# Optimization experiments

Hardware: AMD Instinct MI355X
Metric: run time of the kernel (lower is better)

The kernel has to match this reference:

```python
import jax, jax.numpy as jnp
import numpy as np

B, S, D_MODEL = 2, 2048, 2048
H, DS, DG, DV = 16, 64, 64, 128
ROPE_BASE = 10000.0
NEG_INF = -1e9


def _rope(x, base=ROPE_BASE):
    # x: [B, S, H, D] -> rotate-half RoPE over positions 0..S-1
    d = x.shape[-1]
    half = d // 2
    inv_freq = 1.0 / (base ** (jnp.arange(half, dtype=jnp.float32) / half))
    ang = jnp.arange(x.shape[1], dtype=jnp.float32)[:, None] * inv_freq  # [S, half]
    cos = jnp.cos(ang)[None, :, None, :]
    sin = jnp.sin(ang)[None, :, None, :]
    x1, x2 = x[..., :half], x[..., half:]
    return jnp.concatenate([x1 * cos - x2 * sin, x1 * sin + x2 * cos], axis=-1)


def setup_inputs() -> dict:
    key = jax.random.key(0)
    ks = jax.random.split(key, 8)
    s = lambda fan_in: 1.0 / np.sqrt(fan_in)
    return {
        "x": jax.random.normal(ks[0], (B, S, D_MODEL), dtype=jnp.float32),
        "wq_sem": jax.random.normal(ks[1], (D_MODEL, H * DS), dtype=jnp.float32) * s(D_MODEL),
        "wk_sem": jax.random.normal(ks[2], (D_MODEL, H * DS), dtype=jnp.float32) * s(D_MODEL),
        "wq_geo": jax.random.normal(ks[3], (D_MODEL, H * DG), dtype=jnp.float32) * s(D_MODEL),
        "wk_geo": jax.random.normal(ks[4], (D_MODEL, H * DG), dtype=jnp.float32) * s(D_MODEL),
        "wv": jax.random.normal(ks[5], (D_MODEL, H * DV), dtype=jnp.float32) * s(D_MODEL),
        "wo": jax.random.normal(ks[6], (H * DV, D_MODEL), dtype=jnp.float32) * s(H * DV),
        "gate_logit": jax.random.normal(ks[7], (H,), dtype=jnp.float32),
    }


def reference(x, wq_sem, wk_sem, wq_geo, wk_geo, wv, wo, gate_logit):
    b, sl, _ = x.shape
    # Projections -> [B, S, H, d]
    qs = (x @ wq_sem).reshape(b, sl, H, DS)
    ksem = (x @ wk_sem).reshape(b, sl, H, DS)
    qg = _rope((x @ wq_geo).reshape(b, sl, H, DG))
    kg = _rope((x @ wk_geo).reshape(b, sl, H, DG))
    v = (x @ wv).reshape(b, sl, H, DV)

    sem_scale = 1.0 / np.sqrt(DS)
    geo_scale = 1.0 / np.sqrt(DG)
    sem_scores = jnp.einsum("bqhd,bkhd->bhqk", qs, ksem) * sem_scale
    geo_scores = jnp.einsum("bqhd,bkhd->bhqk", qg, kg) * geo_scale

    # Learned per-head gate mixing semantic vs geometric paths
    g = jax.nn.sigmoid(gate_logit)[None, :, None, None]
    scores = g * sem_scores + (1.0 - g) * geo_scores

    causal = jnp.tril(jnp.ones((sl, sl), dtype=bool))
    scores = jnp.where(causal[None, None], scores, NEG_INF)
    attn = jax.nn.softmax(scores, axis=-1)

    out = jnp.einsum("bhqk,bkhd->bqhd", attn, v).reshape(b, sl, H * DV)
    return out @ wo
```

## Files before the change

### kernel.cpp

```cpp
#include <hip/hip_runtime.h>
#include <hip/hip_bf16.h>

typedef unsigned short u16;
typedef __attribute__((ext_vector_type(4))) float floatx4;
typedef __attribute__((ext_vector_type(8))) __bf16 bf16x8;

__device__ __forceinline__ u16 f2bf(float f) {
  unsigned int x = __builtin_bit_cast(unsigned int, f);
  unsigned int r = (x + 0x7fffu + ((x >> 16) & 1u)) >> 16;
  return (u16)r;
}
__device__ __forceinline__ float bf2f(u16 u) {
  unsigned int x = ((unsigned int)u) << 16;
  return __builtin_bit_cast(float, x);
}
__device__ __forceinline__ floatx4 mfma16(bf16x8 a, bf16x8 b, floatx4 c) {
  return __builtin_amdgcn_mfma_f32_16x16x32_bf16(a, b, c, 0, 0, 0);
}
__device__ __forceinline__ void gload16(const u16* g, u16* l) {
  __builtin_amdgcn_global_load_lds(
      (const __attribute__((address_space(1))) unsigned int*)g,
      (__attribute__((address_space(3))) unsigned int*)l, 16, 0, 0);
}
#define SCHEDB() __builtin_amdgcn_sched_barrier(0)
#define SBAR() __builtin_amdgcn_s_barrier()

#define BB 2
#define SS 2048
#define DM 2048
#define HH 16
#define PCOLS 6144

__global__ void convert_bf16_k(const float* __restrict__ src, u16* __restrict__ dst, size_t n) {
  size_t i = ((size_t)blockIdx.x * blockDim.x + threadIdx.x) * 4;
  if (i + 3 >= n) { for (size_t j = i; j < n; ++j) dst[j] = f2bf(src[j]); return; }
  float4 v = *(const float4*)&src[i];
  ushort4 o; o.x = f2bf(v.x); o.y = f2bf(v.y); o.z = f2bf(v.z); o.w = f2bf(v.w);
  *(ushort4*)&dst[i] = o;
}

__global__ void transpose_all_k(const float* w0, const float* w1, const float* w2,
                                const float* w3, const float* w4, const float* w5,
                                u16* __restrict__ WcatT, u16* __restrict__ WoT) {
  __shared__ float tile[32][33];
  const int z = blockIdx.z;
  const float* src; u16* dst; int cols;
  if (z == 0)      { src = w0; dst = WcatT;                        cols = 1024; }
  else if (z == 1) { src = w1; dst = WcatT + (size_t)1024 * 2048;  cols = 1024; }
  else if (z == 2) { src = w2; dst = WcatT + (size_t)2048 * 2048;  cols = 1024; }
  else if (z == 3) { src = w3; dst = WcatT + (size_t)3072 * 2048;  cols = 1024; }
  else if (z == 4) { src = w4; dst = WcatT + (size_t)4096 * 2048;  cols = 2048; }
  else             { src = w5; dst = WoT;                          cols = 2048; }
  int c0 = blockIdx.x * 32;
  if (c0 >= cols) return;
  int r0 = blockIdx.y * 32;
  int tx = threadIdx.x, ty = threadIdx.y;
#pragma unroll
  for (int i = 0; i < 4; ++i)
    tile[ty + i * 8][tx] = src[(size_t)(r0 + ty + i * 8) * cols + c0 + tx];
  __syncthreads();
#pragma unroll
  for (int i = 0; i < 4; ++i)
    dst[(size_t)(c0 + ty + i * 8) * 2048 + r0 + tx] = f2bf(tile[tx][ty + i * 8]);
}

__global__ void vtrans_k(const u16* __restrict__ P, u16* __restrict__ VtG) {
  __shared__ u16 t[32][33];
  int b = blockIdx.z;
  int c0 = blockIdx.x * 32;
  int s0 = blockIdx.y * 32;
  int tx = threadIdx.x, ty = threadIdx.y;
#pragma unroll
  for (int i = 0; i < 4; ++i)
    t[ty + i * 8][tx] = P[((size_t)b * SS + s0 + ty + i * 8) * PCOLS + 4096 + c0 + tx];
  __syncthreads();
#pragma unroll
  for (int i = 0; i < 4; ++i)
    VtG[((size_t)b * 2048 + c0 + ty + i * 8) * SS + s0 + tx] = t[tx][ty + i * 8];
}

__global__ void rope_table_k(float* __restrict__ cosT, float* __restrict__ sinT) {
  int idx = blockIdx.x * 256 + threadIdx.x;
  int s = idx >> 5, d = idx & 31;
  double inv = pow(10000.0, -(double)d / 32.0);
  double ang = (double)s * inv;
  cosT[idx] = (float)cos(ang);
  sinT[idx] = (float)sin(ang);
}

__global__ void rope_apply_k(u16* __restrict__ P, const float* __restrict__ cosT,
                             const float* __restrict__ sinT) {
  int idx = blockIdx.x * 256 + threadIdx.x;
  int d = idx & 31, h = (idx >> 5) & 15, reg = (idx >> 9) & 1, row = idx >> 10;
  int s = row & (SS - 1);
  size_t base = (size_t)row * PCOLS + (reg ? 3072 : 2048) + h * 64 + d;
  float x1 = bf2f(P[base]), x2 = bf2f(P[base + 32]);
  float c = cosT[s * 32 + d], sn = sinT[s * 32 + d];
  P[base] = f2bf(x1 * c - x2 * sn);
  P[base + 32] = f2bf(x1 * sn + x2 * c);
}

template <bool OUTF32>
__global__ __launch_bounds__(512, 1)
void gemm2_k(const u16* __restrict__ A, const u16* __restrict__ Bt,
             void* __restrict__ Cout, int M, int N, int K) {
  __shared__ alignas(16) u16 lds[49152];
  const int tid = threadIdx.x;
  const int wid = tid >> 6, lane = tid & 63;
  const int lr = lane & 15, lg = lane >> 4;
  const int wr = wid >> 2, wc = wid & 3;
  const int nwgx = gridDim.x;
  const int nwg = nwgx * gridDim.y;
  const int lin = blockIdx.y * nwgx + blockIdx.x;
  const int swz = (lin & 7) * (nwg >> 3) + (lin >> 3);
  const int m0 = (swz / nwgx) * 128, n0 = (swz % nwgx) * 256;
  const int NT = K >> 6;

  const int aoff = lr * 32 + ((lg ^ ((lr >> 1) & 3)) * 8);

  const int srow = tid >> 2;
  const int sgl = (((tid & 3) ^ ((tid >> 3) & 3)) * 8);
  const u16* Asrc = A + (size_t)(m0 + srow) * K + sgl;
  const u16* Bsrc = Bt + (size_t)(n0 + srow) * K + sgl;

  floatx4 acc[4][4];
#pragma unroll
  for (int m = 0; m < 4; ++m)
#pragma unroll
    for (int n = 0; n < 4; ++n) acc[m][n] = (floatx4){0.f, 0.f, 0.f, 0.f};

  auto stage_half = [&](int tile, int kh) {
    if (tile >= NT) return;
    const int rb = (tile & 1) * 2 + kh;
    gload16(Asrc + tile * 64 + kh * 32, lds + rb * 4096 + wid * 512);
    u16* db = lds + 16384 + rb * 8192 + wid * 512;
    const u16* sb = Bsrc + tile * 64 + kh * 32;
    gload16(sb, db);
    gload16(sb + (size_t)128 * K, db + 4096);
  };

  stage_half(0, 0); stage_half(0, 1); stage_half(1, 0);
  asm volatile("s_waitcnt vmcnt(3)" ::: "memory");
  SCHEDB(); SBAR(); SCHEDB();

  bf16x8 af[4], bfv[4];

#pragma unroll 1
  for (int it = 0; it < (NT >> 1); ++it) {
    const int t = it * 2;

#define PH(BUF, KK, STILE, SKH, MORE)                                       \
    {                                                                       \
      const u16* Ab = lds + ((BUF) * 2 + (KK)) * 4096;                      \
      const u16* Bb = lds + 16384 + ((BUF) * 2 + (KK)) * 8192;              \
      _Pragma("unroll") for (int m = 0; m < 4; ++m)                         \
        af[m] = *(const bf16x8*)&Ab[(wr * 64 + m * 16) * 32 + aoff];        \
      _Pragma("unroll") for (int n = 0; n < 4; ++n)                         \
        bfv[n] = *(const bf16x8*)&Bb[(wc * 64 + n * 16) * 32 + aoff];       \
      stage_half((STILE), (SKH));                                           \
      SCHEDB(); SBAR(); SCHEDB();                                           \
      __builtin_amdgcn_s_setprio(1);                                        \
      _Pragma("unroll") for (int m = 0; m < 4; ++m)                         \
        _Pragma("unroll") for (int n = 0; n < 4; ++n)                       \
          acc[m][n] = mfma16(af[m], bfv[n], acc[m][n]);                     \
      __builtin_amdgcn_s_setprio(0);                                        \
      if (MORE) asm volatile("s_waitcnt vmcnt(6)" ::: "memory");            \
      else      asm volatile("s_waitcnt vmcnt(0)" ::: "memory");            \
      SCHEDB(); SBAR(); SCHEDB();                                           \
    }

    PH(0, 0, t + 1, 1, (t + 2 < NT))
    PH(0, 1, t + 2, 0, (t + 2 < NT))
    PH(1, 0, t + 2, 1, (t + 3 < NT))
    PH(1, 1, t + 3, 0, (t + 3 < NT))
#undef PH
  }

#pragma unroll
  for (int m = 0; m < 4; ++m) {
    int row0 = m0 + wr * 64 + m * 16 + lg * 4;
#pragma unroll
    for (int n = 0; n < 4; ++n) {
      int col = n0 + wc * 64 + n * 16 + lr;
#pragma unroll
      for (int r = 0; r < 4; ++r) {
        size_t off = (size_t)(row0 + r) * N + col;
        if (OUTF32) ((float*)Cout)[off] = acc[m][n][r];
        else        ((u16*)Cout)[off] = f2bf(acc[m][n][r]);
      }
    }
  }
}

__device__ __forceinline__ bf16x8 load_scaled(const u16* p, float s) {
  uint4 raw = *(const uint4*)p;
  const u16* ru = (const u16*)&raw;
  bf16x8 out;
#pragma unroll
  for (int j = 0; j < 8; ++j) out[j] = (__bf16)(bf2f(ru[j]) * s);
  return out;
}

__global__ __launch_bounds__(256, 3)
void attn_k(const u16* __restrict__ P, const u16* __restrict__ VtG,
            const float* __restrict__ gate, u16* __restrict__ AttO) {
  const int pairi = blockIdx.x >> 4;
  const int h = blockIdx.x & 15;
  const int b = blockIdx.y;
  const int tid = threadIdx.x, wid = tid >> 6, lane = tid & 63;
  const int lr = lane & 15, lg = lane >> 4;
  const size_t rowb = (size_t)b * SS;

  const float g = 1.f / (1.f + __expf(-gate[h]));
  const float ssc = g * 0.125f;
  const float gsc = (1.f - g) * 0.125f;

  __shared__ alignas(16) u16 Ks[64 * 64];
  __shared__ alignas(16) u16 Kg[64 * 64];
  __shared__ alignas(16) u16 Vt[128 * 64];
  __shared__ alignas(16) u16 Pw[4][16 * 64];

  const int strow = tid >> 3;
  const int stg = ((tid & 7) ^ (strow & 7)) * 8;
  const int swz = lr & 7;

  for (int half = 0; half < 2; ++half) {
    const int qb = half ? (31 - pairi) : pairi;
    const int q0 = qb * 64;

    const u16* qbase = P + (rowb + q0 + wid * 16 + lr) * PCOLS + h * 64;
    bf16x8 qs[2], qg[2];
#pragma unroll
    for (int kk = 0; kk < 2; ++kk) {
      qs[kk] = load_scaled(qbase + kk * 32 + lg * 8, ssc);
      qg[kk] = load_scaled(qbase + 2048 + kk * 32 + lg * 8, gsc);
    }

    float m_r = -1e30f, l_r = 0.f;
    floatx4 o[8];
#pragma unroll
    for (int n = 0; n < 8; ++n) o[n] = (floatx4){0.f, 0.f, 0.f, 0.f};

    const int nkv = q0 + 64;
    for (int kv0 = 0; kv0 < nkv; kv0 += 64) {
      __syncthreads();
      {
        const u16* ks = P + (rowb + kv0 + strow) * PCOLS + 1024 + h * 64 + stg;
        const u16* gs = P + (rowb + kv0 + strow) * PCOLS + 3072 + h * 64 + stg;
        gload16(ks, Ks + wid * 512);
        gload16(gs, Kg + wid * 512);
        gload16(ks + (size_t)32 * PCOLS, Ks + 2048 + wid * 512);
        gload16(gs + (size_t)32 * PCOLS, Kg + 2048 + wid * 512);
      }
      {
        const u16* vs = VtG + ((size_t)b * 2048 + h * 128 + strow) * SS + kv0 + stg;
#pragma unroll
        for (int c = 0; c < 4; ++c)
          gload16(vs + (size_t)(c * 32) * SS, Vt + c * 2048 + wid * 512);
      }
      __syncthreads();

      floatx4 sc[4];
#pragma unroll
      for (int s = 0; s < 4; ++s) sc[s] = (floatx4){0.f, 0.f, 0.f, 0.f};
#pragma unroll
      for (int kk = 0; kk < 2; ++kk) {
#pragma unroll
        for (int s = 0; s < 4; ++s) {
          bf16x8 kf = *(const bf16x8*)&Ks[(s * 16 + lr) * 64 + ((kk * 4 + lg) ^ swz) * 8];
          bf16x8 gf = *(const bf16x8*)&Kg[(s * 16 + lr) * 64 + ((kk * 4 + lg) ^ swz) * 8];
          sc[s] = mfma16(kf, qs[kk], sc[s]);
          sc[s] = mfma16(gf, qg[kk], sc[s]);
        }
      }

      const int qrow = q0 + wid * 16 + lr;
      const bool needmask = (kv0 + 63 > q0 + wid * 16);
      float vv[4][4];
      float vmax = -1e30f;
#pragma unroll
      for (int s = 0; s < 4; ++s)
#pragma unroll
        for (int r = 0; r < 4; ++r) {
          float val = sc[s][r];
          if (needmask) val = (kv0 + s * 16 + lg * 4 + r <= qrow) ? val : -1e30f;
          vv[s][r] = val;
          vmax = fmaxf(vmax, val);
        }
      vmax = fmaxf(vmax, __shfl_xor(vmax, 16));
      vmax = fmaxf(vmax, __shfl_xor(vmax, 32));
      float mnew = fmaxf(m_r, vmax);
      float corr = __expf(m_r - mnew);
      float psum = 0.f;
#pragma unroll
      for (int s = 0; s < 4; ++s)
#pragma unroll
        for (int r = 0; r < 4; ++r) {
          vv[s][r] = __expf(vv[s][r] - mnew);
          psum += vv[s][r];
        }
      psum += __shfl_xor(psum, 16);
      psum += __shfl_xor(psum, 32);
      l_r = l_r * corr + psum;
      m_r = mnew;

#pragma unroll
      for (int s = 0; s < 4; ++s)
#pragma unroll
        for (int t = 0; t < 2; ++t) {
          unsigned int w;
          asm("v_cvt_pk_bf16_f32 %0, %1, %2" : "=v"(w) : "v"(vv[s][2 * t]), "v"(vv[s][2 * t + 1]));
          int u16off = lr * 64 + ((s * 2 + (lg >> 1)) ^ swz) * 8 + (lg & 1) * 4 + t * 2;
          *(unsigned int*)&Pw[wid][u16off] = w;
        }

      float crr[4];
#pragma unroll
      for (int r = 0; r < 4; ++r) crr[r] = __shfl(corr, lg * 4 + r);
#pragma unroll
      for (int n = 0; n < 8; ++n)
#pragma unroll
        for (int r = 0; r < 4; ++r) o[n][r] *= crr[r];

      asm volatile("s_waitcnt lgkmcnt(0)" ::: "memory");
      SCHEDB();
      bf16x8 pa0 = *(const bf16x8*)&Pw[wid][lr * 64 + (lg ^ swz) * 8];
      bf16x8 pa1 = *(const bf16x8*)&Pw[wid][lr * 64 + ((4 + lg) ^ swz) * 8];
#pragma unroll
      for (int n = 0; n < 8; ++n) {
        bf16x8 vb0 = *(const bf16x8*)&Vt[(n * 16 + lr) * 64 + (lg ^ swz) * 8];
        bf16x8 vb1 = *(const bf16x8*)&Vt[(n * 16 + lr) * 64 + ((4 + lg) ^ swz) * 8];
        o[n] = mfma16(pa0, vb0, o[n]);
        o[n] = mfma16(pa1, vb1, o[n]);
      }
    }

    float linv = 1.f / l_r;
    float lnv[4];
#pragma unroll
    for (int r = 0; r < 4; ++r) lnv[r] = __shfl(linv, lg * 4 + r);
#pragma unroll
    for (int n = 0; n < 8; ++n)
#pragma unroll
      for (int r = 0; r < 4; ++r) {
        float val = o[n][r] * lnv[r];
        AttO[(rowb + q0 + wid * 16 + lg * 4 + r) * (size_t)(HH * 128) + h * 128 + n * 16 + lr] =
            f2bf(val);
      }
  }
}

extern "C" void kernel_launch(void* const* d_in, const int* in_sizes, int n_in,
                              void* d_out, int out_size, void* d_ws, size_t ws_size,
                              hipStream_t stream) {
  const float* x       = (const float*)d_in[0];
  const float* wq_sem  = (const float*)d_in[1];
  const float* wk_sem  = (const float*)d_in[2];
  const float* wq_geo  = (const float*)d_in[3];
  const float* wk_geo  = (const float*)d_in[4];
  const float* wv      = (const float*)d_in[5];
  const float* wo      = (const float*)d_in[6];
  const float* gate    = (const float*)d_in[7];

  char* ws = (char*)d_ws;
  u16* Xbf   = (u16*)(ws);
  u16* WcatT = (u16*)(ws + 16777216);
  u16* WoT   = (u16*)(ws + 16777216 + 25165824);
  u16* P     = (u16*)(ws + 16777216 + 25165824 + 8388608);
  float* cosT = (float*)(ws + 16777216 + 25165824 + 8388608 + 50331648);
  float* sinT = cosT + 2048 * 32;
  u16* AttO = Xbf;
  u16* VtG  = WcatT;

  dim3 tb(32, 8);
  convert_bf16_k<<<8192, 256, 0, stream>>>(x, Xbf, (size_t)4096 * 2048);
  transpose_all_k<<<dim3(64, 64, 6), tb, 0, stream>>>(wq_sem, wk_sem, wq_geo, wk_geo,
                                                      wv, wo, WcatT, WoT);
  rope_table_k<<<256, 256, 0, stream>>>(cosT, sinT);

  gemm2_k<false><<<dim3(24, 32), 512, 0, stream>>>(Xbf, WcatT, P, 4096, 6144, 2048);
  rope_apply_k<<<16384, 256, 0, stream>>>(P, cosT, sinT);
  vtrans_k<<<dim3(64, 64, 2), tb, 0, stream>>>(P, VtG);
  attn_k<<<dim3(256, 2), 256, 0, stream>>>(P, VtG, gate, AttO);
  gemm2_k<true><<<dim3(8, 32), 512, 0, stream>>>(AttO, WoT, d_out, 4096, 2048, 2048);
}
```

Measured before the change: 275.7 us.

## Add 256x256-tile GEMM for QKV projection and drop block swizzle

Adds a new GEMM kernel that computes 256x256 output tiles per workgroup with 8x4 MFMA accumulators per wave and a reworked double-buffered LDS staging schedule. It is used for the fused QKV projection, halving the number of workgroups and raising arithmetic intensity per loaded tile. The existing 128x256 GEMM loses its L2-friendly block swizzle and gains an explicit lgkmcnt wait before the MFMAs. The larger tile uses more LDS and registers, and the 384-workgroup grid may leave CUs unevenly loaded in the last wave.

```diff
diff --git a/kernel.cpp b/kernel.cpp
--- a/kernel.cpp
+++ b/kernel.cpp
@@ -102,6 +102,105 @@
 
 template <bool OUTF32>
 __global__ __launch_bounds__(512, 1)
+void gemm256_k(const u16* __restrict__ A, const u16* __restrict__ Bt,
+               void* __restrict__ Cout, int M, int N, int K) {
+  __shared__ alignas(16) u16 lds[65536];
+  const int tid = threadIdx.x;
+  const int wid = tid >> 6, lane = tid & 63;
+  const int lr = lane & 15, lg = lane >> 4;
+  const int wr = wid >> 2, wc = wid & 3;
+  const int m0 = blockIdx.y * 256, n0 = blockIdx.x * 256;
+  const int NT = K >> 6;
+
+  const int aoff = lr * 32 + ((lg ^ ((lr >> 1) & 3)) * 8);
+
+  const int srow = tid >> 2;
+  const int sgl = (((tid & 3) ^ ((tid >> 3) & 3)) * 8);
+  const u16* Asrc = A + (size_t)(m0 + srow) * K + sgl;
+  const u16* Bsrc = Bt + (size_t)(n0 + srow) * K + sgl;
+
+  floatx4 acc[8][4];
+#pragma unroll
+  for (int m = 0; m < 8; ++m)
+#pragma unroll
+    for (int n = 0; n < 4; ++n) acc[m][n] = (floatx4){0.f, 0.f, 0.f, 0.f};
+
+  auto stage = [&](int tile, int h) {
+    if (tile >= NT) return;
+    const int isB = h & 1, kh = h >> 1;
+    const u16* s = (isB ? Bsrc : Asrc) + tile * 64 + kh * 32;
+    u16* d = lds + isB * 32768 + ((tile & 1) * 2 + kh) * 8192 + wid * 512;
+    gload16(s, d);
+    gload16(s + (size_t)128 * K, d + 4096);
+  };
+
+  stage(0, 0); stage(0, 1); stage(0, 2); stage(0, 3);
+  asm volatile("s_waitcnt vmcnt(2)" ::: "memory");
+  SCHEDB(); SBAR(); SCHEDB();
+
+  bf16x8 af[4], bfv[4];
+
+#pragma unroll 1
+  for (int t = 0; t < NT; ++t) {
+    const int buf = t & 1;
+    const u16* A0 = lds + (buf * 2 + 0) * 8192;
+    const u16* A1 = lds + (buf * 2 + 1) * 8192;
+    const u16* B0 = lds + 32768 + (buf * 2 + 0) * 8192;
+    const u16* B1 = lds + 32768 + (buf * 2 + 1) * 8192;
+    const bool more = (t + 1 < NT);
+
+#define PH(AB, BB_, MH, SH, WAITC)                                             \
+    {                                                                          \
+      if ((MH) == 0) {                                                         \
+        _Pragma("unroll") for (int nf = 0; nf < 4; ++nf)                       \
+          bfv[nf] = *(const bf16x8*)&(BB_)[(wc * 64 + nf * 16) * 32 + aoff];   \
+      }                                                                        \
+      _Pragma("unroll") for (int mf = 0; mf < 4; ++mf)                         \
+        af[mf] = *(const bf16x8*)&(AB)[(wr * 128 + ((MH) * 4 + mf) * 16) * 32 + aoff]; \
+      stage(t + 1, SH);                                                        \
+      SCHEDB(); SBAR(); SCHEDB();                                              \
+      asm volatile("s_waitcnt lgkmcnt(0)" ::: "memory");                       \
+      SCHEDB();                                                                \
+      __builtin_amdgcn_s_setprio(1);                                           \
+      _Pragma("unroll") for (int mf = 0; mf < 4; ++mf)                         \
+        _Pragma("unroll") for (int nf = 0; nf < 4; ++nf)                       \
+          acc[(MH) * 4 + mf][nf] = mfma16(af[mf], bfv[nf], acc[(MH) * 4 + mf][nf]); \
+      __builtin_amdgcn_s_setprio(0);                                           \
+      if ((WAITC) == 1) {                                                      \
+        if (more) asm volatile("s_waitcnt vmcnt(4)" ::: "memory");             \
+        else      asm volatile("s_waitcnt vmcnt(0)" ::: "memory");             \
+      } else if ((WAITC) == 2) {                                               \
+        if (more) asm volatile("s_waitcnt vmcnt(2)" ::: "memory");             \
+        else      asm volatile("s_waitcnt vmcnt(0)" ::: "memory");             \
+      }                                                                        \
+      SCHEDB(); SBAR(); SCHEDB();                                              \
+    }
+
+    PH(A0, B0, 0, 0, 0)
+    PH(A0, B0, 1, 1, 1)
+    PH(A1, B1, 0, 2, 0)
+    PH(A1, B1, 1, 3, 2)
+#undef PH
+  }
+
+#pragma unroll
+  for (int m = 0; m < 8; ++m) {
+    int row0 = m0 + wr * 128 + m * 16 + lg * 4;
+#pragma unroll
+    for (int n = 0; n < 4; ++n) {
+      int col = n0 + wc * 64 + n * 16 + lr;
+#pragma unroll
+      for (int r = 0; r < 4; ++r) {
+        size_t off = (size_t)(row0 + r) * N + col;
+        if (OUTF32) ((float*)Cout)[off] = acc[m][n][r];
+        else        ((u16*)Cout)[off] = f2bf(acc[m][n][r]);
+      }
+    }
+  }
+}
+
+template <bool OUTF32>
+__global__ __launch_bounds__(512, 1)
 void gemm2_k(const u16* __restrict__ A, const u16* __restrict__ Bt,
              void* __restrict__ Cout, int M, int N, int K) {
   __shared__ alignas(16) u16 lds[49152];
@@ -109,15 +208,10 @@
   const int wid = tid >> 6, lane = tid & 63;
   const int lr = lane & 15, lg = lane >> 4;
   const int wr = wid >> 2, wc = wid & 3;
-  const int nwgx = gridDim.x;
-  const int nwg = nwgx * gridDim.y;
-  const int lin = blockIdx.y * nwgx + blockIdx.x;
-  const int swz = (lin & 7) * (nwg >> 3) + (lin >> 3);
-  const int m0 = (swz / nwgx) * 128, n0 = (swz % nwgx) * 256;
+  const int m0 = blockIdx.y * 128, n0 = blockIdx.x * 256;
   const int NT = K >> 6;
 
   const int aoff = lr * 32 + ((lg ^ ((lr >> 1) & 3)) * 8);
-
   const int srow = tid >> 2;
   const int sgl = (((tid & 3) ^ ((tid >> 3) & 3)) * 8);
   const u16* Asrc = A + (size_t)(m0 + srow) * K + sgl;
@@ -159,6 +253,8 @@
         bfv[n] = *(const bf16x8*)&Bb[(wc * 64 + n * 16) * 32 + aoff];       \
       stage_half((STILE), (SKH));                                           \
       SCHEDB(); SBAR(); SCHEDB();                                           \
+      asm volatile("s_waitcnt lgkmcnt(0)" ::: "memory");                    \
+      SCHEDB();                                                             \
       __builtin_amdgcn_s_setprio(1);                                        \
       _Pragma("unroll") for (int m = 0; m < 4; ++m)                         \
         _Pragma("unroll") for (int n = 0; n < 4; ++n)                       \
@@ -378,7 +474,7 @@
                                                       wv, wo, WcatT, WoT);
   rope_table_k<<<256, 256, 0, stream>>>(cosT, sinT);
 
-  gemm2_k<false><<<dim3(24, 32), 512, 0, stream>>>(Xbf, WcatT, P, 4096, 6144, 2048);
+  gemm256_k<false><<<dim3(24, 16), 512, 0, stream>>>(Xbf, WcatT, P, 4096, 6144, 2048);
   rope_apply_k<<<16384, 256, 0, stream>>>(P, cosT, sinT);
   vtrans_k<<<dim3(64, 64, 2), tb, 0, stream>>>(P, VtG);
   attn_k<<<dim3(256, 2), 256, 0, stream>>>(P, VtG, gate, AttO);
```

Result: no change. 278.4 us (+1.0%).

## Replace half-tile 4-phase GEMM pipeline with simple full-tile double buffering

Applied to the files above, without the earlier changes.

The GEMM kernel's staging pipeline moves from four half-tile phases, each with its own barrier and staggered prefetch, to a simpler loop. That loop prefetches the whole next K-tile, waits, reads both K-halves from LDS and issues all 32 MFMAs per tile. The XCD-aware block swizzle is also removed in favour of direct blockIdx mapping. This cuts barriers per tile and shortens the code, but exposes LDS read latency before the MFMAs and gives up the L2 locality from the swizzle.

```diff
diff --git a/kernel.cpp b/kernel.cpp
--- a/kernel.cpp
+++ b/kernel.cpp
@@ -102,18 +102,14 @@
 
 template <bool OUTF32>
 __global__ __launch_bounds__(512, 1)
-void gemm2_k(const u16* __restrict__ A, const u16* __restrict__ Bt,
-             void* __restrict__ Cout, int M, int N, int K) {
+void gemm2p_k(const u16* __restrict__ A, const u16* __restrict__ Bt,
+              void* __restrict__ Cout, int M, int N, int K) {
   __shared__ alignas(16) u16 lds[49152];
   const int tid = threadIdx.x;
   const int wid = tid >> 6, lane = tid & 63;
   const int lr = lane & 15, lg = lane >> 4;
   const int wr = wid >> 2, wc = wid & 3;
-  const int nwgx = gridDim.x;
-  const int nwg = nwgx * gridDim.y;
-  const int lin = blockIdx.y * nwgx + blockIdx.x;
-  const int swz = (lin & 7) * (nwg >> 3) + (lin >> 3);
-  const int m0 = (swz / nwgx) * 128, n0 = (swz % nwgx) * 256;
+  const int m0 = blockIdx.y * 128, n0 = blockIdx.x * 256;
   const int NT = K >> 6;
 
   const int aoff = lr * 32 + ((lg ^ ((lr >> 1) & 3)) * 8);
@@ -129,51 +125,63 @@
 #pragma unroll
     for (int n = 0; n < 4; ++n) acc[m][n] = (floatx4){0.f, 0.f, 0.f, 0.f};
 
-  auto stage_half = [&](int tile, int kh) {
+  auto stage_tile = [&](int tile) {
     if (tile >= NT) return;
-    const int rb = (tile & 1) * 2 + kh;
-    gload16(Asrc + tile * 64 + kh * 32, lds + rb * 4096 + wid * 512);
-    u16* db = lds + 16384 + rb * 8192 + wid * 512;
-    const u16* sb = Bsrc + tile * 64 + kh * 32;
-    gload16(sb, db);
-    gload16(sb + (size_t)128 * K, db + 4096);
+    const int buf = tile & 1;
+#pragma unroll
+    for (int kh = 0; kh < 2; ++kh) {
+      const int rb = buf * 2 + kh;
+      gload16(Asrc + tile * 64 + kh * 32, lds + rb * 4096 + wid * 512);
+      u16* db = lds + 16384 + rb * 8192 + wid * 512;
+      const u16* sb = Bsrc + tile * 64 + kh * 32;
+      gload16(sb, db);
+      gload16(sb + (size_t)128 * K, db + 4096);
+    }
   };
 
-  stage_half(0, 0); stage_half(0, 1); stage_half(1, 0);
-  asm volatile("s_waitcnt vmcnt(3)" ::: "memory");
+  stage_tile(0);
+  asm volatile("s_waitcnt vmcnt(0)" ::: "memory");
   SCHEDB(); SBAR(); SCHEDB();
 
-  bf16x8 af[4], bfv[4];
-
 #pragma unroll 1
-  for (int it = 0; it < (NT >> 1); ++it) {
-    const int t = it * 2;
-
-#define PH(BUF, KK, STILE, SKH, MORE)                                       \
-    {                                                                       \
-      const u16* Ab = lds + ((BUF) * 2 + (KK)) * 4096;                      \
-      const u16* Bb = lds + 16384 + ((BUF) * 2 + (KK)) * 8192;              \
-      _Pragma("unroll") for (int m = 0; m < 4; ++m)                         \
-        af[m] = *(const bf16x8*)&Ab[(wr * 64 + m * 16) * 32 + aoff];        \
-      _Pragma("unroll") for (int n = 0; n < 4; ++n)                         \
-        bfv[n] = *(const bf16x8*)&Bb[(wc * 64 + n * 16) * 32 + aoff];       \
-      stage_half((STILE), (SKH));                                           \
-      SCHEDB(); SBAR(); SCHEDB();                                           \
-      __builtin_amdgcn_s_setprio(1);                                        \
-      _Pragma("unroll") for (int m = 0; m < 4; ++m)                         \
-        _Pragma("unroll") for (int n = 0; n < 4; ++n)                       \
-          acc[m][n] = mfma16(af[m], bfv[n], acc[m][n]);                     \
-      __builtin_amdgcn_s_setprio(0);                                        \
-      if (MORE) asm volatile("s_waitcnt vmcnt(6)" ::: "memory");            \
-      else      asm volatile("s_waitcnt vmcnt(0)" ::: "memory");            \
-      SCHEDB(); SBAR(); SCHEDB();                                           \
-    }
-
-    PH(0, 0, t + 1, 1, (t + 2 < NT))
-    PH(0, 1, t + 2, 0, (t + 2 < NT))
-    PH(1, 0, t + 2, 1, (t + 3 < NT))
-    PH(1, 1, t + 3, 0, (t + 3 < NT))
-#undef PH
+  for (int t = 0; t < NT; ++t) {
+    const int buf = t & 1;
+    const u16* A0 = lds + (buf * 2 + 0) * 4096;
+    const u16* A1 = lds + (buf * 2 + 1) * 4096;
+    const u16* B0 = lds + 16384 + (buf * 2 + 0) * 8192;
+    const u16* B1 = lds + 16384 + (buf * 2 + 1) * 8192;
+
+    stage_tile(t + 1);
+    asm volatile("s_waitcnt vmcnt(6)" ::: "memory");
+    SCHEDB(); SBAR(); SCHEDB();
+
+    bf16x8 af0[4], bf0v[4], af1[4], bf1v[4];
+#pragma unroll
+    for (int m = 0; m < 4; ++m)
+      af0[m] = *(const bf16x8*)&A0[(wr * 64 + m * 16) * 32 + aoff];
+#pragma unroll
+    for (int n = 0; n < 4; ++n)
+      bf0v[n] = *(const bf16x8*)&B0[(wc * 64 + n * 16) * 32 + aoff];
+#pragma unroll
+    for (int m = 0; m < 4; ++m)
+      af1[m] = *(const bf16x8*)&A1[(wr * 64 + m * 16) * 32 + aoff];
+#pragma unroll
+    for (int n = 0; n < 4; ++n)
+      bf1v[n] = *(const bf16x8*)&B1[(wc * 64 + n * 16) * 32 + aoff];
+
+    __builtin_amdgcn_s_setprio(1);
+#pragma unroll
+    for (int m = 0; m < 4; ++m)
+#pragma unroll
+      for (int n = 0; n < 4; ++n)
+        acc[m][n] = mfma16(af0[m], bf0v[n], acc[m][n]);
+#pragma unroll
+    for (int m = 0; m < 4; ++m)
+#pragma unroll
+      for (int n = 0; n < 4; ++n)
+        acc[m][n] = mfma16(af1[m], bf1v[n], acc[m][n]);
+    __builtin_amdgcn_s_setprio(0);
+    SCHEDB(); SBAR(); SCHEDB();
   }
 
 #pragma unroll
@@ -378,9 +386,9 @@
                                                       wv, wo, WcatT, WoT);
   rope_table_k<<<256, 256, 0, stream>>>(cosT, sinT);
 
-  gemm2_k<false><<<dim3(24, 32), 512, 0, stream>>>(Xbf, WcatT, P, 4096, 6144, 2048);
+  gemm2p_k<false><<<dim3(24, 32), 512, 0, stream>>>(Xbf, WcatT, P, 4096, 6144, 2048);
   rope_apply_k<<<16384, 256, 0, stream>>>(P, cosT, sinT);
   vtrans_k<<<dim3(64, 64, 2), tb, 0, stream>>>(P, VtG);
   attn_k<<<dim3(256, 2), 256, 0, stream>>>(P, VtG, gate, AttO);
-  gemm2_k<true><<<dim3(8, 32), 512, 0, stream>>>(AttO, WoT, d_out, 4096, 2048, 2048);
-}
+  gemm2p_k<true><<<dim3(8, 32), 512, 0, stream>>>(AttO, WoT, d_out, 4096, 2048, 2048);
+}
```

Result: slower. 284.1 us (+3.1%).
